# Performance work log

Measured on AMD Instinct MI355X. Metric: run time of the kernel, lower is better.

## Reference

```python
import jax, jax.numpy as jnp
import numpy as np

B, T, D, H, E, R, M, HID, NB = 8, 832, 1024, 16, 16, 8, 16, 4096, 576
LORA_SCALE = 1.0 / R  # alpha / rank


def _ln(x, g, b, eps=1e-6):
    m = x.mean(-1, keepdims=True)
    v = ((x - m) ** 2).mean(-1, keepdims=True)
    return (x - m) / jnp.sqrt(v + eps) * g + b


def setup_inputs() -> dict:
    key = jax.random.key(0)
    ks = jax.random.split(key, 12)
    sd = 0.02
    return {
        's': jax.random.normal(ks[0], (B, T, D), jnp.float32),
        'attn_mask': jnp.zeros((1, 1, T, T), jnp.float32),
        'g1': jnp.ones((D,), jnp.float32),
        'b1': jnp.zeros((D,), jnp.float32),
        'w_qkv': jax.random.normal(ks[1], (D, 3 * D), jnp.float32) * sd,
        'b_qkv': jnp.zeros((3 * D,), jnp.float32),
        'w_proj': jax.random.normal(ks[2], (D, D), jnp.float32) * sd,
        'b_proj': jnp.zeros((D,), jnp.float32),
        'g2': jnp.ones((D,), jnp.float32),
        'b2': jnp.zeros((D,), jnp.float32),
        'w_fc1': jax.random.normal(ks[3], (D, HID), jnp.float32) * sd,
        'b_fc1': jnp.zeros((HID,), jnp.float32),
        'w_fc2': jax.random.normal(ks[4], (HID, D), jnp.float32) * sd,
        'b_fc2': jnp.zeros((D,), jnp.float32),
        'lora_A': jax.random.normal(ks[5], (E, D, R), jnp.float32) * sd,
        'lora_B': jax.random.normal(ks[6], (E, R, D), jnp.float32) * sd,
        'active_expert_indices': jnp.arange(E, dtype=jnp.int32),
        'num_backbone_tokens': NB,
    }


def reference(s, attn_mask, g1, b1, w_qkv, b_qkv, w_proj, b_proj,
              g2, b2, w_fc1, b_fc1, w_fc2, b_fc2, lora_A, lora_B,
              active_expert_indices, num_backbone_tokens):
    Bb, Tt, Dd = s.shape
    hd = Dd // H
    # --- shared attention ---
    x = _ln(s, g1, b1)
    qkv = (x @ w_qkv + b_qkv).reshape(Bb, Tt, 3, H, hd).transpose(2, 0, 3, 1, 4)
    q, k, v = qkv[0], qkv[1], qkv[2]  # [B,H,T,hd]
    scores = jnp.einsum('bhqd,bhkd->bhqk', q * (hd ** -0.5), k) + attn_mask
    p = jax.nn.softmax(scores, axis=-1)
    o = jnp.einsum('bhqk,bhkd->bhqd', p, v).transpose(0, 2, 1, 3).reshape(Bb, Tt, Dd)
    s = s + (o @ w_proj + b_proj)
    # --- shared MLP ---
    s_norm = _ln(s, g2, b2)
    shared = jax.nn.gelu(s_norm @ w_fc1 + b_fc1, approximate=False) @ w_fc2 + b_fc2
    # --- per-expert LoRA on expert token segment ---
    nb = num_backbone_tokens
    z = s_norm[:, nb:, :].reshape(Bb, -1, M, Dd)  # [B,K,M,D]
    Ak = lora_A[active_expert_indices]            # [K,D,R]
    Bk = lora_B[active_expert_indices]            # [K,R,D]
    down = jnp.einsum('bkmd,kdr->bkmr', z, Ak)
    up = jnp.einsum('bkmr,krd->bkmd', down, Bk) * LORA_SCALE
    shared = shared.at[:, nb:, :].add(up.reshape(Bb, -1, Dd))
    return s + shared
```

## Files before the change

### kernel.cpp

```cpp
#include <hip/hip_runtime.h>
#include <hip/hip_bf16.h>
#include <math.h>

typedef unsigned short u16;
typedef __attribute__((ext_vector_type(8))) short short8;
typedef __attribute__((ext_vector_type(4))) float f32x4;

constexpr int B_ = 8, T_ = 832, D_ = 1024, H_ = 16, HID_ = 4096, NB_ = 576;
constexpr int NT_ = B_ * T_;

__device__ inline u16 f2b(float f) {
    union { float f; unsigned u; } x{f};
    unsigned r = (x.u + 0x7FFFu + ((x.u >> 16) & 1u)) >> 16;
    return (u16)r;
}
__device__ inline float b2f(u16 b) {
    union { unsigned u; float f; } x; x.u = ((unsigned)b) << 16; return x.f;
}

__device__ inline float erf_inl(float x) {
    float ax = fabsf(x);
    float t = __frcp_rn(1.0f + 0.3275911f * ax);
    float p = 1.061405429f;
    p = p * t - 1.453152027f;
    p = p * t + 1.421413741f;
    p = p * t - 0.284496736f;
    p = p * t + 0.254829592f;
    p = p * t;
    float e = 1.0f - p * __expf(-ax * ax);
    return copysignf(e, x);
}

__device__ inline void gload_lds16(const void* g, void* l) {
    __builtin_amdgcn_global_load_lds((const __attribute__((address_space(1))) void*)g,
                                     (__attribute__((address_space(3))) void*)l, 16, 0, 0);
}

__global__ __launch_bounds__(256) void wtrans_all(const float* __restrict__ wq,
                                                  const float* __restrict__ wp,
                                                  const float* __restrict__ w1,
                                                  const float* __restrict__ w2,
                                                  u16* __restrict__ oq, u16* __restrict__ op,
                                                  u16* __restrict__ o1, u16* __restrict__ o2) {
    __shared__ u16 tile[32][34];
    int bid = blockIdx.x;
    const float* in; u16* out; int K, N, idx;
    if (bid < 3072)      { in = wq; out = oq; K = 1024; N = 3072; idx = bid; }
    else if (bid < 4096) { in = wp; out = op; K = 1024; N = 1024; idx = bid - 3072; }
    else if (bid < 8192) { in = w1; out = o1; K = 1024; N = 4096; idx = bid - 4096; }
    else                 { in = w2; out = o2; K = 4096; N = 1024; idx = bid - 8192; }
    int nx = N >> 5;
    int n0 = (idx % nx) * 32, k0 = (idx / nx) * 32;
    int tx = threadIdx.x & 31, ty = threadIdx.x >> 5;
    for (int i = 0; i < 4; i++) {
        int k = k0 + ty + i * 8;
        tile[ty + i * 8][tx] = f2b(in[(size_t)k * N + n0 + tx]);
    }
    __syncthreads();
    for (int i = 0; i < 4; i++) {
        int n = n0 + ty + i * 8;
        out[(size_t)n * K + k0 + tx] = tile[tx][ty + i * 8];
    }
}

__global__ __launch_bounds__(256) void ln_kernel(const float* __restrict__ x,
                                                 const float* __restrict__ g,
                                                 const float* __restrict__ bt,
                                                 u16* __restrict__ out) {
    int row = blockIdx.x, tid = threadIdx.x;
    float4 v = ((const float4*)(x + (size_t)row * D_))[tid];
    float s = v.x + v.y + v.z + v.w;
    float q = v.x * v.x + v.y * v.y + v.z * v.z + v.w * v.w;
    for (int o = 1; o < 64; o <<= 1) { s += __shfl_xor(s, o); q += __shfl_xor(q, o); }
    __shared__ float red[4][2];
    if ((tid & 63) == 0) { red[tid >> 6][0] = s; red[tid >> 6][1] = q; }
    __syncthreads();
    s = red[0][0] + red[1][0] + red[2][0] + red[3][0];
    q = red[0][1] + red[1][1] + red[2][1] + red[3][1];
    float mean = s * (1.0f / D_);
    float var = q * (1.0f / D_) - mean * mean;
    float inv = rsqrtf(fmaxf(var, 0.f) + 1e-6f);
    float4 gv = ((const float4*)g)[tid];
    float4 bv = ((const float4*)bt)[tid];
    u16* orow = out + (size_t)row * D_ + tid * 4;
    orow[0] = f2b((v.x - mean) * inv * gv.x + bv.x);
    orow[1] = f2b((v.y - mean) * inv * gv.y + bv.y);
    orow[2] = f2b((v.z - mean) * inv * gv.z + bv.z);
    orow[3] = f2b((v.w - mean) * inv * gv.w + bv.w);
}

template<int BM, int BN, int WR, int WC, int MODE>
__global__ __launch_bounds__(WR * WC * 64, (WR * WC == 8) ? 2 : 3)
void gemm3(const u16* __restrict__ A, const u16* __restrict__ Bt,
           const float* __restrict__ bias, const float* __restrict__ resid,
           void* __restrict__ outp, int M, int N, int K) {
    constexpr int THREADS = WR * WC * 64;
    constexpr int MF = BM / WR / 16;
    constexpr int NF = BN / WC / 16;
    constexpr int NROWS = BM + BN;
    constexpr int CHUNKS = NROWS * 4 / THREADS;
    constexpr int LDSU = NROWS * 32;
    __shared__ u16 lds_[3 * LDSU];

    int tid = threadIdx.x, l = tid & 63, w = tid >> 6;
    int lrow = l & 15, lgrp = l >> 4;
    int wr = w / WC, wc = w % WC;

    int nwg = gridDim.x * gridDim.y;
    int bid = blockIdx.y * gridDim.x + blockIdx.x;
    int cpx = nwg >> 3;
    int swz = (bid & 7) * cpx + (bid >> 3);
    int bx = swz % gridDim.x, by = swz / gridDim.x;
    int m0 = by * BM, n0 = bx * BN;

    const u16* src[CHUNKS];
    int ldst[CHUNKS];
#pragma unroll
    for (int i = 0; i < CHUNKS; i++) {
        int c = i * THREADS + tid;
        int lc = (c & ~7) | ((c ^ (c >> 3)) & 7);
        int row = lc >> 2, colu = (lc & 3) * 8;
        src[i] = (row < BM) ? A + (size_t)(m0 + row) * K + colu
                            : Bt + (size_t)(n0 + row - BM) * K + colu;
        ldst[i] = c * 8;
    }

#define STAGE3(bufi, kt)                                                    \
    do {                                                                    \
        int kof = (kt) * 32;                                                \
        u16* bb = lds_ + (bufi) * LDSU;                                     \
        _Pragma("unroll")                                                   \
        for (int i = 0; i < CHUNKS; i++) gload_lds16(src[i] + kof, bb + ldst[i]); \
    } while (0)

    f32x4 acc[MF][NF];
#pragma unroll
    for (int m = 0; m < MF; m++)
#pragma unroll
        for (int n = 0; n < NF; n++) acc[m][n] = (f32x4){0, 0, 0, 0};

    int aidx[MF], bidx[NF];
#pragma unroll
    for (int m = 0; m < MF; m++) {
        int row = wr * 64 + m * 16 + lrow;
        aidx[m] = (row * 32 + lgrp * 8) ^ (((row >> 1) & 7) << 3);
    }
#pragma unroll
    for (int n = 0; n < NF; n++) {
        int row = BM + wc * 64 + n * 16 + lrow;
        bidx[n] = (row * 32 + lgrp * 8) ^ (((row >> 1) & 7) << 3);
    }

    int nkt = K >> 5;
    STAGE3(0, 0);
    STAGE3(1, 1);
    if constexpr (CHUNKS == 3) asm volatile("s_waitcnt vmcnt(3)" ::: "memory");
    else                       asm volatile("s_waitcnt vmcnt(4)" ::: "memory");
    asm volatile("s_barrier" ::: "memory");

    int cur = 0;
    for (int t = 0; t < nkt; ++t) {
        int sb = cur + 2; if (sb >= 3) sb -= 3;
        if (t + 2 < nkt) STAGE3(sb, t + 2);

        const u16* bp = lds_ + cur * LDSU;
        short8 af[MF], bfr[NF];
#pragma unroll
        for (int m = 0; m < MF; m++) af[m] = *(const short8*)(bp + aidx[m]);
#pragma unroll
        for (int n = 0; n < NF; n++) bfr[n] = *(const short8*)(bp + bidx[n]);

        __builtin_amdgcn_s_setprio(1);
#pragma unroll
        for (int m = 0; m < MF; m++)
#pragma unroll
            for (int n = 0; n < NF; n++)
                acc[m][n] = __builtin_amdgcn_mfma_f32_16x16x32_bf16(af[m], bfr[n], acc[m][n], 0, 0, 0);
        __builtin_amdgcn_s_setprio(0);

        if (t + 2 < nkt) {
            if constexpr (CHUNKS == 3) asm volatile("s_waitcnt vmcnt(3)" ::: "memory");
            else                       asm volatile("s_waitcnt vmcnt(4)" ::: "memory");
        } else if (t + 1 < nkt) {
            asm volatile("s_waitcnt vmcnt(0)" ::: "memory");
        }
        asm volatile("s_barrier" ::: "memory");
        cur = cur + 1; if (cur == 3) cur = 0;
    }
#undef STAGE3

#pragma unroll
    for (int m = 0; m < MF; m++) {
        int rbase = m0 + wr * 64 + m * 16 + lgrp * 4;
#pragma unroll
        for (int n = 0; n < NF; n++) {
            int col = n0 + wc * 64 + n * 16 + lrow;
            float bv = bias[col];
#pragma unroll
            for (int j = 0; j < 4; j++) {
                int row = rbase + j;
                float v = acc[m][n][j] + bv;
                size_t off = (size_t)row * N + col;
                if constexpr (MODE == 0) {
                    ((u16*)outp)[off] = f2b(v);
                } else if constexpr (MODE == 1) {
                    ((float*)outp)[off] = v + resid[off];
                } else {
                    float gl = 0.5f * v * (1.0f + erf_inl(v * 0.70710678118654752f));
                    ((u16*)outp)[off] = f2b(gl);
                }
            }
        }
    }
}

__global__ __launch_bounds__(256) void vtrans_kernel(const u16* __restrict__ qkv,
                                                     u16* __restrict__ vt) {
    __shared__ u16 tile[32][66];
    int bh = blockIdx.y, b = bh >> 4, h = bh & 15;
    int t0 = blockIdx.x * 32;
    int dx = threadIdx.x & 63, ty = threadIdx.x >> 6;
    for (int i = 0; i < 8; i++) {
        int tt = ty * 8 + i;
        tile[tt][dx] = qkv[(size_t)(b * T_ + t0 + tt) * 3072 + 2048 + h * 64 + dx];
    }
    __syncthreads();
    int tx = threadIdx.x & 31, dy = threadIdx.x >> 5;
    for (int i = 0; i < 8; i++) {
        int d = dy * 8 + i;
        vt[((size_t)bh * 64 + d) * T_ + t0 + tx] = tile[tx][d];
    }
}

__global__ __launch_bounds__(512, 4) void attn_kernel(const u16* __restrict__ qkv,
                                                      const u16* __restrict__ vt,
                                                      const float* __restrict__ mask,
                                                      u16* __restrict__ obuf) {
    __shared__ u16 Ks[2][4096];
    __shared__ u16 Vs[2][4096];
    __shared__ u16 Ps[8][1024];
    int qt = blockIdx.x, bh = blockIdx.y, b = bh >> 4, h = bh & 15;
    int tid = threadIdx.x, w = tid >> 6, l = tid & 63;
    int lrow = l & 15, lgrp = l >> 4;

    int qrow = qt * 128 + w * 16 + lrow;
    int qrc = qrow < T_ ? qrow : T_ - 1;
    const u16* qp = qkv + (size_t)(b * T_ + qrc) * 3072 + h * 64 + lgrp * 8;
    short8 aq0, aq1;
    {
        short8 r0 = *(const short8*)qp;
        short8 r1 = *(const short8*)(qp + 32);
        for (int i = 0; i < 8; i++) {
            aq0[i] = (short)f2b(b2f((u16)r0[i]) * 0.125f);
            aq1[i] = (short)f2b(b2f((u16)r1[i]) * 0.125f);
        }
    }

    int tq0 = qt * 128 + w * 16 + lgrp * 4;
    bool qvalid = tq0 < T_;
    const float* mrowp[4];
#pragma unroll
    for (int j = 0; j < 4; j++) {
        int tq = tq0 + j; if (tq >= T_) tq = T_ - 1;
        mrowp[j] = mask + (size_t)tq * T_;
    }

    float m_r[4], l_r[4];
    f32x4 oacc[4];
    for (int j = 0; j < 4; j++) { m_r[j] = -1e30f; l_r[j] = 0.f; }
    for (int n = 0; n < 4; n++) oacc[n] = (f32x4){0, 0, 0, 0};

    int srow = tid >> 3, sp = tid & 7;
    int se = (sp ^ (srow & 7)) * 8;
    const u16* kbase = qkv + (size_t)b * T_ * 3072 + 1024 + h * 64;
    const u16* vbase = vt + (size_t)bh * 64 * T_;

#define STAGE_KV(buf, kk0)                                                        \
    do {                                                                          \
        gload_lds16(kbase + (size_t)((kk0) + srow) * 3072 + se, &Ks[buf][w * 512]); \
        gload_lds16(vbase + (size_t)srow * T_ + (kk0) + se, &Vs[buf][w * 512]);     \
    } while (0)

    float mc[16], mn[16];
    STAGE_KV(0, 0);
#pragma unroll
    for (int j = 0; j < 4; j++)
#pragma unroll
        for (int c = 0; c < 4; c++)
            mc[j * 4 + c] = mrowp[j][c * 16 + lrow];
    __syncthreads();

    int cur = 0;
    u16* Pw = Ps[w];
    int swl = lrow & 7;
    int slot0 = (lgrp ^ swl) * 8, slot1 = ((lgrp + 4) ^ swl) * 8;

    for (int kt = 0; kt < 13; ++kt) {
        int kk0 = kt * 64;
        if (kt < 12) {
            STAGE_KV(cur ^ 1, kk0 + 64);
#pragma unroll
            for (int j = 0; j < 4; j++)
#pragma unroll
                for (int c = 0; c < 4; c++)
                    mn[j * 4 + c] = mrowp[j][kk0 + 64 + c * 16 + lrow];
        }

        f32x4 sc[4];
        for (int c = 0; c < 4; c++) sc[c] = (f32x4){0, 0, 0, 0};
        const u16* Kb = Ks[cur];
        __builtin_amdgcn_s_setprio(1);
        for (int c = 0; c < 4; c++) {
            const u16* krow = Kb + (c * 16 + lrow) * 64;
            short8 bk0 = *(const short8*)(krow + slot0);
            short8 bk1 = *(const short8*)(krow + slot1);
            sc[c] = __builtin_amdgcn_mfma_f32_16x16x32_bf16(aq0, bk0, sc[c], 0, 0, 0);
            sc[c] = __builtin_amdgcn_mfma_f32_16x16x32_bf16(aq1, bk1, sc[c], 0, 0, 0);
        }
        __builtin_amdgcn_s_setprio(0);

        int lo3 = lrow & 7, hi = lrow >> 3;
#pragma unroll
        for (int j = 0; j < 4; j++) {
            float s0 = sc[0][j] + mc[j * 4 + 0];
            float s1 = sc[1][j] + mc[j * 4 + 1];
            float s2 = sc[2][j] + mc[j * 4 + 2];
            float s3 = sc[3][j] + mc[j * 4 + 3];
            float mx = fmaxf(fmaxf(s0, s1), fmaxf(s2, s3));
            mx = fmaxf(mx, __shfl_xor(mx, 1));
            mx = fmaxf(mx, __shfl_xor(mx, 2));
            mx = fmaxf(mx, __shfl_xor(mx, 4));
            mx = fmaxf(mx, __shfl_xor(mx, 8));
            float mnew = fmaxf(m_r[j], mx);
            float scf = __expf(m_r[j] - mnew);
            float p0 = __expf(s0 - mnew), p1 = __expf(s1 - mnew);
            float p2 = __expf(s2 - mnew), p3 = __expf(s3 - mnew);
            float ps = (p0 + p1) + (p2 + p3);
            ps += __shfl_xor(ps, 1); ps += __shfl_xor(ps, 2);
            ps += __shfl_xor(ps, 4); ps += __shfl_xor(ps, 8);
            l_r[j] = l_r[j] * scf + ps;
            m_r[j] = mnew;
            for (int n = 0; n < 4; n++) oacc[n][j] *= scf;
            int row_p = lgrp * 4 + j, swp = row_p & 7;
            u16* pr = Pw + row_p * 64;
            pr[((hi ^ swp) * 8) + lo3]       = f2b(p0);
            pr[(((2 + hi) ^ swp) * 8) + lo3] = f2b(p1);
            pr[(((4 + hi) ^ swp) * 8) + lo3] = f2b(p2);
            pr[(((6 + hi) ^ swp) * 8) + lo3] = f2b(p3);
        }

        short8 ap0 = *(const short8*)&Pw[lrow * 64 + slot0];
        short8 ap1 = *(const short8*)&Pw[lrow * 64 + slot1];
        const u16* Vb = Vs[cur];
        __builtin_amdgcn_s_setprio(1);
        for (int n = 0; n < 4; n++) {
            const u16* vrow = Vb + (n * 16 + lrow) * 64;
            short8 bv0 = *(const short8*)(vrow + slot0);
            short8 bv1 = *(const short8*)(vrow + slot1);
            oacc[n] = __builtin_amdgcn_mfma_f32_16x16x32_bf16(ap0, bv0, oacc[n], 0, 0, 0);
            oacc[n] = __builtin_amdgcn_mfma_f32_16x16x32_bf16(ap1, bv1, oacc[n], 0, 0, 0);
        }
        __builtin_amdgcn_s_setprio(0);

        __syncthreads();
#pragma unroll
        for (int i = 0; i < 16; i++) mc[i] = mn[i];
        cur ^= 1;
    }
#undef STAGE_KV

    if (qvalid) {
        for (int j = 0; j < 4; j++) {
            float inv = 1.0f / l_r[j];
            int t = tq0 + j;
            for (int n = 0; n < 4; n++)
                obuf[(size_t)(b * T_ + t) * 1024 + h * 64 + n * 16 + lrow] = f2b(oacc[n][j] * inv);
        }
    }
}

__global__ __launch_bounds__(256) void lora_kernel(const u16* __restrict__ snorm,
                                                   const float* __restrict__ lA,
                                                   const float* __restrict__ lB,
                                                   const int* __restrict__ idx,
                                                   float* __restrict__ outp) {
    __shared__ float down[16][8];
    int blk = blockIdx.x, b = blk >> 4, kk = blk & 15;
    int e = idx[kk];
    int tok0 = b * T_ + NB_ + kk * 16;
    int tid = threadIdx.x;
    {
        int m = tid >> 4;
        int r = (tid >> 1) & 7;
        int dh = tid & 1;
        const u16* z = snorm + (size_t)(tok0 + m) * D_ + dh * 512;
        const float* Ae = lA + (size_t)e * D_ * 8 + (size_t)(dh * 512) * 8 + r;
        float acc = 0.f;
        for (int d = 0; d < 512; ++d) acc += b2f(z[d]) * Ae[(size_t)d * 8];
        acc += __shfl_xor(acc, 1);
        if (dh == 0) down[m][r] = acc;
    }
    __syncthreads();
    for (int ci = 0; ci < 4; ci++) {
        int col = tid + ci * 256;
        float br[8];
        for (int r = 0; r < 8; r++) br[r] = lB[((size_t)e * 8 + r) * D_ + col];
        for (int m = 0; m < 16; m++) {
            float acc = 0.f;
            for (int r = 0; r < 8; r++) acc += down[m][r] * br[r];
            outp[(size_t)(tok0 + m) * D_ + col] += acc * 0.125f;
        }
    }
}

extern "C" void kernel_launch(void* const* d_in, const int* in_sizes, int n_in,
                              void* d_out, int out_size, void* d_ws, size_t ws_size,
                              hipStream_t stream) {
    const float* s      = (const float*)d_in[0];
    const float* mask   = (const float*)d_in[1];
    const float* g1     = (const float*)d_in[2];
    const float* b1     = (const float*)d_in[3];
    const float* w_qkv  = (const float*)d_in[4];
    const float* b_qkv  = (const float*)d_in[5];
    const float* w_proj = (const float*)d_in[6];
    const float* b_proj = (const float*)d_in[7];
    const float* g2     = (const float*)d_in[8];
    const float* b2     = (const float*)d_in[9];
    const float* w_fc1  = (const float*)d_in[10];
    const float* b_fc1  = (const float*)d_in[11];
    const float* w_fc2  = (const float*)d_in[12];
    const float* b_fc2  = (const float*)d_in[13];
    const float* lA     = (const float*)d_in[14];
    const float* lB     = (const float*)d_in[15];
    const int*   eidx   = (const int*)d_in[16];
    float* out = (float*)d_out;
    char* ws = (char*)d_ws;

    u16*   wqkvT = (u16*)(ws + 0);
    u16*   wprojT= (u16*)(ws + 6291456);
    u16*   wfc1T = (u16*)(ws + 8388608);
    u16*   wfc2T = (u16*)(ws + 16777216);
    float* s1    = (float*)(ws + 25165824);
    u16*   xln   = (u16*)(ws + 52428800);
    u16*   vt    = (u16*)(ws + 66060288);
    u16*   qkv   = (u16*)(ws + 79691776);
    u16*   h     = (u16*)(ws + 66060288);

    wtrans_all<<<12288, 256, 0, stream>>>(w_qkv, w_proj, w_fc1, w_fc2,
                                          wqkvT, wprojT, wfc1T, wfc2T);
    ln_kernel<<<NT_, 256, 0, stream>>>(s, g1, b1, xln);
    gemm3<128, 256, 2, 4, 0><<<dim3(3072 / 256, NT_ / 128), 512, 0, stream>>>(xln, wqkvT, b_qkv, nullptr, qkv, NT_, 3072, 1024);
    vtrans_kernel<<<dim3(26, 128), 256, 0, stream>>>(qkv, vt);
    attn_kernel<<<dim3(7, 128), 512, 0, stream>>>(qkv, vt, mask, xln);
    gemm3<128, 128, 2, 2, 1><<<dim3(1024 / 128, NT_ / 128), 256, 0, stream>>>(xln, wprojT, b_proj, s, s1, NT_, 1024, 1024);
    ln_kernel<<<NT_, 256, 0, stream>>>(s1, g2, b2, xln);
    gemm3<128, 256, 2, 4, 2><<<dim3(4096 / 256, NT_ / 128), 512, 0, stream>>>(xln, wfc1T, b_fc1, nullptr, h, NT_, 4096, 1024);
    gemm3<128, 128, 2, 2, 1><<<dim3(1024 / 128, NT_ / 128), 256, 0, stream>>>(h, wfc2T, b_fc2, s1, out, NT_, 1024, 4096);
    lora_kernel<<<128, 256, 0, stream>>>(xln, lA, lB, eidx, out);
}
```

Baseline: 412.0 us.

## Add 256x256-tile double-buffered GEMM kernel for QKV and FC1 projections

Introduces a new gemm5 kernel with 256x256 output tiles, BK=64, XOR-swizzled LDS layout, double buffering, and an XCD-aware block swizzle. It is used for the QKV and FC1 GEMMs, which previously used 128x256 tiles. Larger tiles raise arithmetic intensity and cut global loads per FLOP. The cost is 128 KB of LDS and heavy accumulator register use, which may limit occupancy. The grid is also smaller, 26 row tiles instead of 52, which risks tail imbalance across CUs.

```diff
diff --git a/kernel.cpp b/kernel.cpp
--- a/kernel.cpp
+++ b/kernel.cpp
@@ -87,6 +87,111 @@
     orow[1] = f2b((v.y - mean) * inv * gv.y + bv.y);
     orow[2] = f2b((v.z - mean) * inv * gv.z + bv.z);
     orow[3] = f2b((v.w - mean) * inv * gv.w + bv.w);
+}
+
+template<int MODE>
+__global__ __launch_bounds__(512, 2)
+void gemm5(const u16* __restrict__ A, const u16* __restrict__ Bt,
+           const float* __restrict__ bias, void* __restrict__ outp,
+           int M, int N, int K) {
+    __shared__ u16 lds5[2][32768];
+    int tid = threadIdx.x, l = tid & 63, w = tid >> 6;
+    int lrow = l & 15, lgrp = l >> 4;
+    int wr = w >> 2, wc = w & 3;
+
+    int nwg = gridDim.x * gridDim.y;
+    int bid = blockIdx.y * gridDim.x + blockIdx.x;
+    int cpx = nwg >> 3;
+    int swz = (bid & 7) * cpx + (bid >> 3);
+    int bx = swz % gridDim.x, by = swz / gridDim.x;
+    int m0 = by * 256, n0 = bx * 256;
+
+    const u16* src[8];
+    int ldst[8];
+#pragma unroll
+    for (int i = 0; i < 8; i++) {
+        int c = i * 512 + tid;
+        int row = (c & 2047) >> 3;
+        int ls = (c & 7) ^ (row & 7);
+        src[i] = (c < 2048 ? A + (size_t)(m0 + row) * K : Bt + (size_t)(n0 + row) * K) + ls * 8;
+        ldst[i] = c * 8;
+    }
+
+#define STAGE5(bufi, t)                                                      \
+    do {                                                                     \
+        int ko = (t) * 64;                                                   \
+        u16* bb = &lds5[bufi][0];                                            \
+        _Pragma("unroll")                                                    \
+        for (int i = 0; i < 8; i++) gload_lds16(src[i] + ko, bb + ldst[i]);  \
+    } while (0)
+
+    f32x4 acc[8][4];
+#pragma unroll
+    for (int m = 0; m < 8; m++)
+#pragma unroll
+        for (int n = 0; n < 4; n++) acc[m][n] = (f32x4){0, 0, 0, 0};
+
+    int sw = lrow & 7;
+    int slot0 = (lgrp ^ sw) * 8, slot1 = ((4 + lgrp) ^ sw) * 8;
+    int arow[8], brow[4];
+#pragma unroll
+    for (int m = 0; m < 8; m++) arow[m] = (wr * 128 + m * 16 + lrow) * 64;
+#pragma unroll
+    for (int n = 0; n < 4; n++) brow[n] = 16384 + (wc * 64 + n * 16 + lrow) * 64;
+
+    int nkt = K >> 6;
+    STAGE5(0, 0);
+    asm volatile("s_waitcnt vmcnt(0)" ::: "memory");
+    asm volatile("s_barrier" ::: "memory");
+
+    for (int t = 0; t < nkt; ++t) {
+        int ct = t & 1;
+        if (t + 1 < nkt) STAGE5(ct ^ 1, t + 1);
+        const u16* bp = &lds5[ct][0];
+#pragma unroll
+        for (int kh = 0; kh < 2; kh++) {
+            int so = kh ? slot1 : slot0;
+            short8 bf[4];
+#pragma unroll
+            for (int n = 0; n < 4; n++) bf[n] = *(const short8*)(bp + brow[n] + so);
+#pragma unroll
+            for (int mg = 0; mg < 2; mg++) {
+                short8 af[4];
+#pragma unroll
+                for (int mi = 0; mi < 4; mi++) af[mi] = *(const short8*)(bp + arow[mg * 4 + mi] + so);
+#pragma unroll
+                for (int mi = 0; mi < 4; mi++)
+#pragma unroll
+                    for (int n = 0; n < 4; n++)
+                        acc[mg * 4 + mi][n] =
+                            __builtin_amdgcn_mfma_f32_16x16x32_bf16(af[mi], bf[n], acc[mg * 4 + mi][n], 0, 0, 0);
+            }
+        }
+        if (t + 1 < nkt) asm volatile("s_waitcnt vmcnt(0)" ::: "memory");
+        asm volatile("s_barrier" ::: "memory");
+    }
+#undef STAGE5
+
+#pragma unroll
+    for (int m = 0; m < 8; m++) {
+        int rb = m0 + wr * 128 + m * 16 + lgrp * 4;
+#pragma unroll
+        for (int n = 0; n < 4; n++) {
+            int col = n0 + wc * 64 + n * 16 + lrow;
+            float bv = bias[col];
+#pragma unroll
+            for (int j = 0; j < 4; j++) {
+                float v = acc[m][n][j] + bv;
+                size_t off = (size_t)(rb + j) * N + col;
+                if constexpr (MODE == 0) {
+                    ((u16*)outp)[off] = f2b(v);
+                } else {
+                    float gl = 0.5f * v * (1.0f + erf_inl(v * 0.70710678118654752f));
+                    ((u16*)outp)[off] = f2b(gl);
+                }
+            }
+        }
+    }
 }
 
 template<int BM, int BN, int WR, int WC, int MODE>
@@ -449,12 +554,12 @@
     wtrans_all<<<12288, 256, 0, stream>>>(w_qkv, w_proj, w_fc1, w_fc2,
                                           wqkvT, wprojT, wfc1T, wfc2T);
     ln_kernel<<<NT_, 256, 0, stream>>>(s, g1, b1, xln);
-    gemm3<128, 256, 2, 4, 0><<<dim3(3072 / 256, NT_ / 128), 512, 0, stream>>>(xln, wqkvT, b_qkv, nullptr, qkv, NT_, 3072, 1024);
+    gemm5<0><<<dim3(3072 / 256, NT_ / 256), 512, 0, stream>>>(xln, wqkvT, b_qkv, qkv, NT_, 3072, 1024);
     vtrans_kernel<<<dim3(26, 128), 256, 0, stream>>>(qkv, vt);
     attn_kernel<<<dim3(7, 128), 512, 0, stream>>>(qkv, vt, mask, xln);
     gemm3<128, 128, 2, 2, 1><<<dim3(1024 / 128, NT_ / 128), 256, 0, stream>>>(xln, wprojT, b_proj, s, s1, NT_, 1024, 1024);
     ln_kernel<<<NT_, 256, 0, stream>>>(s1, g2, b2, xln);
-    gemm3<128, 256, 2, 4, 2><<<dim3(4096 / 256, NT_ / 128), 512, 0, stream>>>(xln, wfc1T, b_fc1, nullptr, h, NT_, 4096, 1024);
+    gemm5<2><<<dim3(4096 / 256, NT_ / 256), 512, 0, stream>>>(xln, wfc1T, b_fc1, h, NT_, 4096, 1024);
     gemm3<128, 128, 2, 2, 1><<<dim3(1024 / 128, NT_ / 128), 256, 0, stream>>>(h, wfc2T, b_fc2, s1, out, NT_, 1024, 4096);
     lora_kernel<<<128, 256, 0, stream>>>(xln, lA, lB, eidx, out);
 }
```

After: 403.0 us, median of 3. 2.2% less time.
